# Performance work log

Measured on AMD Instinct MI355X. Metric: run time of the kernel, lower is better.

The kernel has to match this reference:

```python
import jax, jax.numpy as jnp
import numpy as np


def setup_inputs() -> dict:
    key = jax.random.key(0)
    k1, k2 = jax.random.split(key)
    hidden = jax.random.normal(k1, (32, 4096, 768), dtype=jnp.float32)
    querys = jax.random.normal(k2, (1, 768), dtype=jnp.float32)
    return {"hidden": hidden, "querys": querys}


def reference(hidden, querys):
    # scores: [B, S] = hidden @ querys^T (single query)
    scores = jnp.einsum("bsh,qh->bsq", hidden, querys)[..., 0]  # [B, S]
    attn = jax.nn.softmax(scores, axis=-1)                      # [B, S]
    # weighted sum over sequence: [B, H]
    result = jnp.einsum("bs,bsh->bh", attn, hidden)
    return result
```

## Files before the change

### kernel.cpp

```cpp
#include <hip/hip_runtime.h>
#include <math.h>

#define BATCH 32
#define SEQ   4096
#define HID   768
#define HV4   (HID / 4)
#define CHUNKS 64
#define ROWS_PER_BLOCK (SEQ / CHUNKS)
#define NWAVES 4
#define ROWS_PER_WAVE (ROWS_PER_BLOCK / NWAVES)
#define RGROUP 4

typedef __attribute__((ext_vector_type(4))) float f4v;

__device__ __forceinline__ float dot4(f4v a, f4v b) {
  return a.x * b.x + a.y * b.y + a.z * b.z + a.w * b.w;
}

__global__ __launch_bounds__(256, 4)
void attn_pass1(const float* __restrict__ hidden,
                const float* __restrict__ q,
                float* __restrict__ m_ws,
                float* __restrict__ l_ws,
                float* __restrict__ o_ws) {
  const int chunk = blockIdx.x;
  const int b     = blockIdx.y;
  const int tid   = threadIdx.x;
  const int wave  = tid >> 6;
  const int lane  = tid & 63;

  const f4v* q4 = reinterpret_cast<const f4v*>(q);
  const f4v qa = q4[lane];
  const f4v qb = q4[lane + 64];
  const f4v qc = q4[lane + 128];

  float m = -INFINITY;
  float l = 0.0f;
  f4v oa = (f4v)0.0f;
  f4v ob = (f4v)0.0f;
  f4v oc = (f4v)0.0f;

  const int row0 = chunk * ROWS_PER_BLOCK + wave * ROWS_PER_WAVE;
  const f4v* base = reinterpret_cast<const f4v*>(hidden)
                  + ((size_t)b * SEQ + (size_t)row0) * HV4;

  for (int g = 0; g < ROWS_PER_WAVE; g += RGROUP) {
    f4v ra[RGROUP], rb[RGROUP], rc[RGROUP];
    #pragma unroll
    for (int r = 0; r < RGROUP; ++r) {
      const f4v* rp = base + (size_t)(g + r) * HV4;
      ra[r] = __builtin_nontemporal_load(rp + lane);
      rb[r] = __builtin_nontemporal_load(rp + lane + 64);
      rc[r] = __builtin_nontemporal_load(rp + lane + 128);
    }

    float pd[RGROUP];
    #pragma unroll
    for (int r = 0; r < RGROUP; ++r)
      pd[r] = dot4(ra[r], qa) + dot4(rb[r], qb) + dot4(rc[r], qc);

    #pragma unroll
    for (int off = 32; off >= 1; off >>= 1) {
      #pragma unroll
      for (int r = 0; r < RGROUP; ++r)
        pd[r] += __shfl_xor(pd[r], off, 64);
    }

    const float gm = fmaxf(fmaxf(pd[0], pd[1]), fmaxf(pd[2], pd[3]));
    if (gm > m) {
      const float a = __expf(m - gm);
      l *= a;
      oa *= a; ob *= a; oc *= a;
      m = gm;
    }

    #pragma unroll
    for (int r = 0; r < RGROUP; ++r) {
      const float p = __expf(pd[r] - m);
      l += p;
      oa += p * ra[r];
      ob += p * rb[r];
      oc += p * rc[r];
    }
  }

  __shared__ float s_o[NWAVES][HID];
  __shared__ float s_m[NWAVES];
  __shared__ float s_l[NWAVES];
  f4v* so4 = reinterpret_cast<f4v*>(s_o[wave]);
  so4[lane]       = oa;
  so4[lane + 64]  = ob;
  so4[lane + 128] = oc;
  if (lane == 0) { s_m[wave] = m; s_l[wave] = l; }
  __syncthreads();

  const float mb = fmaxf(fmaxf(s_m[0], s_m[1]), fmaxf(s_m[2], s_m[3]));
  const float a0 = __expf(s_m[0] - mb);
  const float a1 = __expf(s_m[1] - mb);
  const float a2 = __expf(s_m[2] - mb);
  const float a3 = __expf(s_m[3] - mb);
  const float lb = a0 * s_l[0] + a1 * s_l[1] + a2 * s_l[2] + a3 * s_l[3];

  const int pidx = b * CHUNKS + chunk;
  float* O = o_ws + (size_t)pidx * HID;
  #pragma unroll
  for (int j = 0; j < 3; ++j) {
    const int h = tid + 256 * j;
    O[h] = a0 * s_o[0][h] + a1 * s_o[1][h] + a2 * s_o[2][h] + a3 * s_o[3][h];
  }
  if (tid == 0) { m_ws[pidx] = mb; l_ws[pidx] = lb; }
}

__global__ __launch_bounds__(128)
void attn_pass2(const float* __restrict__ m_ws,
                const float* __restrict__ l_ws,
                const float* __restrict__ o_ws,
                float* __restrict__ out) {
  const int b = blockIdx.x;
  const int h = blockIdx.y * 128 + threadIdx.x;

  float mg = -INFINITY;
  #pragma unroll 8
  for (int c = 0; c < CHUNKS; ++c)
    mg = fmaxf(mg, m_ws[b * CHUNKS + c]);

  float L = 0.0f;
  float acc = 0.0f;
  #pragma unroll 8
  for (int c = 0; c < CHUNKS; ++c) {
    const int pi = b * CHUNKS + c;
    const float a = __expf(m_ws[pi] - mg);
    L += a * l_ws[pi];
    acc += a * o_ws[(size_t)pi * HID + h];
  }
  out[(size_t)b * HID + h] = acc / L;
}

extern "C" void kernel_launch(void* const* d_in, const int* in_sizes, int n_in,
                              void* d_out, int out_size, void* d_ws, size_t ws_size,
                              hipStream_t stream) {
  const float* hidden = (const float*)d_in[0];
  const float* q      = (const float*)d_in[1];
  float* out = (float*)d_out;

  float* m_ws = (float*)d_ws;
  float* l_ws = m_ws + BATCH * CHUNKS;
  float* o_ws = l_ws + BATCH * CHUNKS;

  dim3 grid1(CHUNKS, BATCH);
  attn_pass1<<<grid1, 256, 0, stream>>>(hidden, q, m_ws, l_ws, o_ws);
  dim3 grid2(BATCH, HID / 128);
  attn_pass2<<<grid2, 128, 0, stream>>>(m_ws, l_ws, o_ws, out);
}
```

Baseline: 498.2 us.

## Double-buffer hidden tiles into LDS with async global_load_lds copies

```diff
diff --git a/kernel.cpp b/kernel.cpp
--- a/kernel.cpp
+++ b/kernel.cpp
@@ -8,8 +8,11 @@
 #define CHUNKS 64
 #define ROWS_PER_BLOCK (SEQ / CHUNKS)
 #define NWAVES 4
-#define ROWS_PER_WAVE (ROWS_PER_BLOCK / NWAVES)
-#define RGROUP 4
+#define TROWS 8
+#define NT    (ROWS_PER_BLOCK / TROWS)
+#define TILE_F4 (TROWS * HV4)
+#define WAVE_F4 (TILE_F4 / NWAVES)
+#define CALLS   (WAVE_F4 / 64)
 
 typedef __attribute__((ext_vector_type(4))) float f4v;
 
@@ -17,12 +20,22 @@
   return a.x * b.x + a.y * b.y + a.z * b.z + a.w * b.w;
 }
 
-__global__ __launch_bounds__(256, 4)
+__device__ __forceinline__ void async_copy16(const f4v* g, f4v* l) {
+  __builtin_amdgcn_global_load_lds(
+      (const __attribute__((address_space(1))) void*)g,
+      (__attribute__((address_space(3))) void*)l,
+      16, 0, 0);
+}
+
+__global__ __launch_bounds__(256, 3)
 void attn_pass1(const float* __restrict__ hidden,
                 const float* __restrict__ q,
                 float* __restrict__ m_ws,
                 float* __restrict__ l_ws,
                 float* __restrict__ o_ws) {
+  __shared__ float lds[2][TROWS * HID];
+  __shared__ float s_m[NWAVES], s_l[NWAVES];
+
   const int chunk = blockIdx.x;
   const int b     = blockIdx.y;
   const int tid   = threadIdx.x;
@@ -34,59 +47,76 @@
   const f4v qb = q4[lane + 64];
   const f4v qc = q4[lane + 128];
 
+  const f4v* gbase = reinterpret_cast<const f4v*>(hidden)
+                   + ((size_t)b * SEQ + (size_t)chunk * ROWS_PER_BLOCK) * HV4;
+  f4v* l0 = reinterpret_cast<f4v*>(lds[0]);
+  f4v* l1 = reinterpret_cast<f4v*>(lds[1]);
+  const int si = wave * WAVE_F4 + lane;
+
+  #pragma unroll
+  for (int c = 0; c < CALLS; ++c)
+    async_copy16(gbase + 0 * TILE_F4 + si + c * 64, l0 + si + c * 64);
+  #pragma unroll
+  for (int c = 0; c < CALLS; ++c)
+    async_copy16(gbase + 1 * TILE_F4 + si + c * 64, l1 + si + c * 64);
+
   float m = -INFINITY;
   float l = 0.0f;
   f4v oa = (f4v)0.0f;
   f4v ob = (f4v)0.0f;
   f4v oc = (f4v)0.0f;
 
-  const int row0 = chunk * ROWS_PER_BLOCK + wave * ROWS_PER_WAVE;
-  const f4v* base = reinterpret_cast<const f4v*>(hidden)
-                  + ((size_t)b * SEQ + (size_t)row0) * HV4;
+  #pragma unroll
+  for (int t = 0; t < NT; ++t) {
+    f4v* lb = (t & 1) ? l1 : l0;
 
-  for (int g = 0; g < ROWS_PER_WAVE; g += RGROUP) {
-    f4v ra[RGROUP], rb[RGROUP], rc[RGROUP];
+    __builtin_amdgcn_sched_barrier(0);
+    if (t < NT - 1) asm volatile("s_waitcnt vmcnt(6)" ::: "memory");
+    else            asm volatile("s_waitcnt vmcnt(0)" ::: "memory");
+    __builtin_amdgcn_s_barrier();
+    __builtin_amdgcn_sched_barrier(0);
+
+    const f4v* r0 = lb + (size_t)(2 * wave + 0) * HV4;
+    const f4v* r1 = lb + (size_t)(2 * wave + 1) * HV4;
+    const f4v a0 = r0[lane], b0 = r0[lane + 64], c0 = r0[lane + 128];
+    const f4v a1 = r1[lane], b1 = r1[lane + 64], c1 = r1[lane + 128];
+
+    float p0 = dot4(a0, qa) + dot4(b0, qb) + dot4(c0, qc);
+    float p1 = dot4(a1, qa) + dot4(b1, qb) + dot4(c1, qc);
     #pragma unroll
-    for (int r = 0; r < RGROUP; ++r) {
-      const f4v* rp = base + (size_t)(g + r) * HV4;
-      ra[r] = __builtin_nontemporal_load(rp + lane);
-      rb[r] = __builtin_nontemporal_load(rp + lane + 64);
-      rc[r] = __builtin_nontemporal_load(rp + lane + 128);
+    for (int off = 32; off >= 1; off >>= 1) {
+      p0 += __shfl_xor(p0, off, 64);
+      p1 += __shfl_xor(p1, off, 64);
     }
 
-    float pd[RGROUP];
-    #pragma unroll
-    for (int r = 0; r < RGROUP; ++r)
-      pd[r] = dot4(ra[r], qa) + dot4(rb[r], qb) + dot4(rc[r], qc);
-
-    #pragma unroll
-    for (int off = 32; off >= 1; off >>= 1) {
-      #pragma unroll
-      for (int r = 0; r < RGROUP; ++r)
-        pd[r] += __shfl_xor(pd[r], off, 64);
-    }
-
-    const float gm = fmaxf(fmaxf(pd[0], pd[1]), fmaxf(pd[2], pd[3]));
+    const float gm = fmaxf(p0, p1);
     if (gm > m) {
       const float a = __expf(m - gm);
       l *= a;
       oa *= a; ob *= a; oc *= a;
       m = gm;
     }
+    const float e0 = __expf(p0 - m);
+    const float e1 = __expf(p1 - m);
+    l += e0 + e1;
+    oa += e0 * a0 + e1 * a1;
+    ob += e0 * b0 + e1 * b1;
+    oc += e0 * c0 + e1 * c1;
 
-    #pragma unroll
-    for (int r = 0; r < RGROUP; ++r) {
-      const float p = __expf(pd[r] - m);
-      l += p;
-      oa += p * ra[r];
-      ob += p * rb[r];
-      oc += p * rc[r];
+    asm volatile("s_waitcnt lgkmcnt(0)" ::: "memory");
+    __builtin_amdgcn_sched_barrier(0);
+    __builtin_amdgcn_s_barrier();
+    __builtin_amdgcn_sched_barrier(0);
+
+    if (t + 2 < NT) {
+      #pragma unroll
+      for (int c = 0; c < CALLS; ++c)
+        async_copy16(gbase + (size_t)(t + 2) * TILE_F4 + si + c * 64,
+                     lb + si + c * 64);
     }
   }
 
-  __shared__ float s_o[NWAVES][HID];
-  __shared__ float s_m[NWAVES];
-  __shared__ float s_l[NWAVES];
+  float (*s_o)[HID] = reinterpret_cast<float(*)[HID]>(lds[0]);
   f4v* so4 = reinterpret_cast<f4v*>(s_o[wave]);
   so4[lane]       = oa;
   so4[lane + 64]  = ob;
@@ -95,20 +125,20 @@
   __syncthreads();
 
   const float mb = fmaxf(fmaxf(s_m[0], s_m[1]), fmaxf(s_m[2], s_m[3]));
-  const float a0 = __expf(s_m[0] - mb);
-  const float a1 = __expf(s_m[1] - mb);
-  const float a2 = __expf(s_m[2] - mb);
-  const float a3 = __expf(s_m[3] - mb);
-  const float lb = a0 * s_l[0] + a1 * s_l[1] + a2 * s_l[2] + a3 * s_l[3];
+  const float w0 = __expf(s_m[0] - mb);
+  const float w1 = __expf(s_m[1] - mb);
+  const float w2 = __expf(s_m[2] - mb);
+  const float w3 = __expf(s_m[3] - mb);
+  const float lsum = w0 * s_l[0] + w1 * s_l[1] + w2 * s_l[2] + w3 * s_l[3];
 
   const int pidx = b * CHUNKS + chunk;
   float* O = o_ws + (size_t)pidx * HID;
   #pragma unroll
   for (int j = 0; j < 3; ++j) {
     const int h = tid + 256 * j;
-    O[h] = a0 * s_o[0][h] + a1 * s_o[1][h] + a2 * s_o[2][h] + a3 * s_o[3][h];
+    O[h] = w0 * s_o[0][h] + w1 * s_o[1][h] + w2 * s_o[2][h] + w3 * s_o[3][h];
   }
-  if (tid == 0) { m_ws[pidx] = mb; l_ws[pidx] = lb; }
+  if (tid == 0) { m_ws[pidx] = mb; l_ws[pidx] = lsum; }
 }
 
 __global__ __launch_bounds__(128)
```

Result: slower. 526.6 us (+5.7%).
